# Kernel optimization log

Hardware: AMD Instinct MI355X
Metric: run time of the kernel (lower is better)

## Reference

```python
import jax, jax.numpy as jnp
import numpy as np

B, LQ, LK, H, DK, DV, E = 4, 1024, 1024, 12, 64, 768, 768
TOPK = 64
TEMP = 0.5
NEG = -10000.0


def setup_inputs() -> dict:
    key = jax.random.key(0)
    ks = jax.random.split(key, 10)
    s = 0.02  # weight init scale
    return {
        "q": jax.random.normal(ks[0], (B, LQ, E), jnp.float32),
        "k": jax.random.normal(ks[1], (B, LK, E), jnp.float32),
        "v": jax.random.normal(ks[2], (B, LK, DV), jnp.float32),
        "qpos": jnp.zeros((B, LQ), jnp.int32),
        "kpos": jnp.zeros((B, LK), jnp.int32),
        "qk_mask": jax.random.normal(ks[3], (B, 1, LQ, LK), jnp.float32) * 0.1,
        "k_mask": jax.random.normal(ks[4], (B, 1, LK, 1), jnp.float32) * 0.1,
        "post_softmax_mask": (jax.random.uniform(ks[5], (B, 1, LQ, LK)) > 0.1).astype(jnp.float32),
        "w_qs": jax.random.normal(ks[6], (E, H * DK), jnp.float32) * s,
        "w_ks": jax.random.normal(ks[7], (E, H * DK), jnp.float32) * s,
        "w_vs": jax.random.normal(ks[8], (DV, H * DV), jnp.float32) * s,
        "fc": jax.random.normal(ks[9], (H * DV, DV), jnp.float32) * s,
    }


def reference(q, k, v, qpos, kpos, qk_mask, k_mask, post_softmax_mask, w_qs, w_ks, w_vs, fc):
    residual = v
    # project and split heads: [b, len, h, d] -> [b, h, len, d]
    qh = (q @ w_qs).reshape(B, LQ, H, DK).transpose(0, 2, 1, 3)
    kh = (k @ w_ks).reshape(B, LK, H, DK).transpose(0, 2, 1, 3)
    vh = (v @ w_vs).reshape(B, LK, H, DV).transpose(0, 2, 1, 3)

    # scaled dot-product scores [b, h, lq, lk]
    attn = jnp.einsum('bhqd,bhkd->bhqk', qh / np.float32(np.sqrt(DK)), kh)
    attn = attn + qk_mask                              # additive qk mask
    attn = attn + jnp.squeeze(k_mask, -1)[:, :, None, :]  # additive key mask

    # topk sparsification: keep top-k scores, fill rest with -10000
    topk_vals, topk_idx = jax.lax.top_k(attn, TOPK)
    attn = jnp.put_along_axis(jnp.full_like(attn, NEG), topk_idx, topk_vals,
                              axis=-1, inplace=False)

    # temperature + stable softmax in fp32
    attn = attn / max(TEMP, 1e-6)
    attn = jax.nn.softmax(attn.astype(jnp.float32), axis=-1).astype(v.dtype)

    # post-softmax multiplicative mask + renorm (renorm_post_mask=True)
    attn = attn * post_softmax_mask
    attn = attn / jnp.maximum(attn.sum(axis=-1, keepdims=True), 1e-6)

    # straight-through argmax hardening (use_argmax=True)
    hard = jax.nn.one_hot(jnp.argmax(attn, axis=-1), LK, dtype=attn.dtype)
    attn = hard - jax.lax.stop_gradient(attn) + attn

    # attend, merge heads, output projection + residual (dropout=0)
    head_output = jnp.einsum('bhqk,bhkd->bhqd', attn, vh)
    output = head_output.transpose(0, 2, 1, 3).reshape(B, LQ, H * DV) @ fc
    output = output + residual
    return (output, attn)
```

## Files before the change

kernel.cpp:

```cpp
#include <hip/hip_runtime.h>

constexpr int NB  = 4;
constexpr int NH  = 12;
constexpr int SEQ = 1024;
constexpr int DKd = 64;
constexpr int DVd = 768;
constexpr int Ed  = 768;
constexpr int HVd = 9216;

typedef float f32x4 __attribute__((ext_vector_type(4)));
typedef short s16x8 __attribute__((ext_vector_type(8)));

__device__ __forceinline__ unsigned short f2bf(float f) {
  unsigned int u = __builtin_bit_cast(unsigned int, f);
  u += 0x7fffu + ((u >> 16) & 1u);
  return (unsigned short)(u >> 16);
}

__device__ __forceinline__ float bf2f_lo(unsigned int u) {
  return __builtin_bit_cast(float, u << 16);
}
__device__ __forceinline__ float bf2f_hi(unsigned int u) {
  return __builtin_bit_cast(float, u & 0xffff0000u);
}

__device__ __forceinline__ f32x4 mfma_bf16_16x16x32(s16x8 a, s16x8 b, f32x4 c) {
  asm("v_mfma_f32_16x16x32_bf16 %0, %1, %2, %0" : "+v"(c) : "v"(a), "v"(b));
  return c;
}

#define GLOAD16(g, l)                                                          \
  __builtin_amdgcn_global_load_lds(                                            \
      (const __attribute__((address_space(1))) unsigned int*)(g),              \
      (__attribute__((address_space(3))) unsigned int*)(l), 16, 0, 0)

__global__ __launch_bounds__(256)
void cvt_bf16_kernel(const float* __restrict__ v, unsigned short* __restrict__ Vbf, int n4) {
  int i = blockIdx.x * 256 + threadIdx.x;
  const int stride = gridDim.x * 256;
  for (; i < n4; i += stride) {
    const f32x4 x = *(const f32x4*)&v[(size_t)i * 4];
    uint2 u;
    u.x = (unsigned)f2bf(x[0]) | ((unsigned)f2bf(x[1]) << 16);
    u.y = (unsigned)f2bf(x[2]) | ((unsigned)f2bf(x[3]) << 16);
    *(uint2*)&Vbf[(size_t)i * 4] = u;
  }
}

__global__ __launch_bounds__(256)
void maskprep_kernel(const float* __restrict__ qk, const float* __restrict__ km,
                     const float* __restrict__ pm, float* __restrict__ ms) {
  const int i = blockIdx.x * 256 + threadIdx.x;
  const int kk4 = i & 255;
  const int b = i >> 18;
  const f32x4 qv = *(const f32x4*)&qk[(size_t)i * 4];
  const f32x4 pv = *(const f32x4*)&pm[(size_t)i * 4];
  const f32x4 kv = *(const f32x4*)&km[b * SEQ + kk4 * 4];
  f32x4 o;
#pragma unroll
  for (int c = 0; c < 4; c++) o[c] = pv[c] > 0.f ? qv[c] + kv[c] : -3.0e38f;
  *(f32x4*)&ms[(size_t)i * 4] = o;
}

__global__ __launch_bounds__(256)
void qkproj_kernel(const float* __restrict__ q, const float* __restrict__ k,
                   const float* __restrict__ w_qs, const float* __restrict__ w_ks,
                   float* __restrict__ qh, float* __restrict__ kh) {
  const float* A  = blockIdx.z ? k : q;
  const float* Bw = blockIdx.z ? w_ks : w_qs;
  float* C        = blockIdx.z ? kh : qh;
  __shared__ float As[16][128];
  __shared__ float Bs[16][128];
  const int tid = threadIdx.x;
  const int bx = (int)blockIdx.x;
  const int sx = ((bx & 7) << 2) | (bx >> 3);
  const int m0 = sx * 128, n0 = blockIdx.y * 128;
  const int ty = tid >> 4, tx = tid & 15;
  const int arow = tid >> 1, akc = (tid & 1) * 8;
  const int bkr = tid >> 4, bnc = (tid & 15) * 8;

  float acc[8][8];
#pragma unroll
  for (int i = 0; i < 8; i++)
#pragma unroll
    for (int j = 0; j < 8; j++) acc[i][j] = 0.f;

  for (int k0 = 0; k0 < 768; k0 += 16) {
    const f32x4 av0 = *(const f32x4*)&A[(size_t)(m0 + arow) * 768 + k0 + akc];
    const f32x4 av1 = *(const f32x4*)&A[(size_t)(m0 + arow) * 768 + k0 + akc + 4];
    const f32x4 bv0 = *(const f32x4*)&Bw[(size_t)(k0 + bkr) * 768 + n0 + bnc];
    const f32x4 bv1 = *(const f32x4*)&Bw[(size_t)(k0 + bkr) * 768 + n0 + bnc + 4];
    __syncthreads();
#pragma unroll
    for (int c = 0; c < 4; c++) {
      As[akc + c][arow]     = av0[c];
      As[akc + 4 + c][arow] = av1[c];
    }
    *(f32x4*)&Bs[bkr][bnc]     = bv0;
    *(f32x4*)&Bs[bkr][bnc + 4] = bv1;
    __syncthreads();
#pragma unroll
    for (int kk = 0; kk < 16; kk++) {
      const f32x4 a0 = *(const f32x4*)&As[kk][ty * 8];
      const f32x4 a1 = *(const f32x4*)&As[kk][ty * 8 + 4];
      const f32x4 b0 = *(const f32x4*)&Bs[kk][tx * 8];
      const f32x4 b1 = *(const f32x4*)&Bs[kk][tx * 8 + 4];
#pragma unroll
      for (int i = 0; i < 4; i++)
#pragma unroll
        for (int j = 0; j < 4; j++) {
          acc[i][j]         += a0[i] * b0[j];
          acc[i][j + 4]     += a0[i] * b1[j];
          acc[i + 4][j]     += a1[i] * b0[j];
          acc[i + 4][j + 4] += a1[i] * b1[j];
        }
    }
  }
#pragma unroll
  for (int i = 0; i < 8; i++) {
    f32x4 o0, o1;
#pragma unroll
    for (int c = 0; c < 4; c++) { o0[c] = acc[i][c]; o1[c] = acc[i][4 + c]; }
    const size_t rb = (size_t)(m0 + ty * 8 + i) * 768 + n0 + tx * 8;
    *(f32x4*)&C[rb] = o0;
    *(f32x4*)&C[rb + 4] = o1;
  }
}

__global__ __launch_bounds__(256)
void score_argmax_kernel(const float* __restrict__ qh, const float* __restrict__ kh,
                         const float* __restrict__ ms, float2* __restrict__ partials) {
  __shared__ float QsT[64][128];
  __shared__ float KsT[64][128];
  const int bh = blockIdx.z;
  const int b = bh / NH, h = bh % NH;
  const int q0 = blockIdx.y * 128;
  const int k0 = blockIdx.x * 128;
  const int tid = threadIdx.x;
  const int ty = tid >> 4, tx = tid & 15;

  const int row = tid >> 1;
  const int cb = (tid & 1) * 32;
  const float* qsrc = qh + (size_t)(b * SEQ + q0 + row) * Ed + h * DKd + cb;
  const float* ksrc = kh + (size_t)(b * SEQ + k0 + row) * Ed + h * DKd + cb;
#pragma unroll
  for (int i = 0; i < 8; i++) {
    const f32x4 qv = *(const f32x4*)&qsrc[4 * i];
    const f32x4 kv = *(const f32x4*)&ksrc[4 * i];
#pragma unroll
    for (int c = 0; c < 4; c++) {
      QsT[cb + 4 * i + c][row] = qv[c];
      KsT[cb + 4 * i + c][row] = kv[c];
    }
  }
  __syncthreads();

  float acc[8][8];
#pragma unroll
  for (int i = 0; i < 8; i++)
#pragma unroll
    for (int j = 0; j < 8; j++) acc[i][j] = 0.f;

#pragma unroll 8
  for (int kk = 0; kk < 64; kk++) {
    const f32x4 a0 = *(const f32x4*)&QsT[kk][ty * 8];
    const f32x4 a1 = *(const f32x4*)&QsT[kk][ty * 8 + 4];
    const f32x4 b0 = *(const f32x4*)&KsT[kk][tx * 8];
    const f32x4 b1 = *(const f32x4*)&KsT[kk][tx * 8 + 4];
#pragma unroll
    for (int i = 0; i < 4; i++)
#pragma unroll
      for (int j = 0; j < 4; j++) {
        acc[i][j]         += a0[i] * b0[j];
        acc[i][j + 4]     += a0[i] * b1[j];
        acc[i + 4][j]     += a1[i] * b0[j];
        acc[i + 4][j + 4] += a1[i] * b1[j];
      }
  }

  const int kg0 = k0 + tx * 8;
#pragma unroll
  for (int i = 0; i < 8; i++) {
    const int qg = q0 + ty * 8 + i;
    const size_t base = (size_t)(b * SEQ + qg) * SEQ + kg0;
    const f32x4 ms0 = *(const f32x4*)&ms[base];
    const f32x4 ms1 = *(const f32x4*)&ms[base + 4];
    float bv = -3.0e38f;
    int bi = 0;
#pragma unroll
    for (int j = 0; j < 4; j++) {
      const float s = acc[i][j] * 0.125f + ms0[j];
      if (s > bv) { bv = s; bi = kg0 + j; }
    }
#pragma unroll
    for (int j = 0; j < 4; j++) {
      const float s = acc[i][4 + j] * 0.125f + ms1[j];
      if (s > bv) { bv = s; bi = kg0 + 4 + j; }
    }
#pragma unroll
    for (int off = 1; off < 16; off <<= 1) {
      const float ov = __shfl_xor(bv, off);
      const int   oi = __shfl_xor(bi, off);
      if (ov > bv || (ov == bv && oi < bi)) { bv = ov; bi = oi; }
    }
    if (tx == 0)
      partials[(size_t)(bh * SEQ + qg) * 8 + blockIdx.x] =
          make_float2(bv, __int_as_float(bi));
  }
}

__global__ __launch_bounds__(256)
void argmax_reduce_kernel(const float2* __restrict__ partials, int* __restrict__ kmaxp) {
  const int t = blockIdx.x * 256 + threadIdx.x;
  if (t >= NB * NH * SEQ) return;
  const float2* p = partials + (size_t)t * 8;
  float bv = -3.0e38f;
  int bi = 0;
#pragma unroll
  for (int i = 0; i < 8; i++) {
    const float vv = p[i].x;
    const int ii = __float_as_int(p[i].y);
    if (vv > bv) { bv = vv; bi = ii; }
  }
  kmaxp[t] = bi;
}

__global__ __launch_bounds__(256)
void wvfc_gemm_kernel(const float* __restrict__ wvs, const float* __restrict__ fcw,
                      unsigned short* __restrict__ MstbT) {
  __shared__ unsigned short As[128][72];
  __shared__ unsigned short Bs[128][72];
  const int tid = threadIdx.x;
  const int h = blockIdx.z;
  const int m0 = blockIdx.x * 128, n0 = blockIdx.y * 128;
  const int wid = tid >> 6, lane = tid & 63;
  const int wr = (wid >> 1) * 64, wc = (wid & 1) * 64;
  const int lm = lane & 15, lq = lane >> 4;
  const int ar = tid >> 1, acb = (tid & 1) * 32;
  const int br = tid >> 2, bnb = (tid & 3) * 32;

  f32x4 acc[4][4];
#pragma unroll
  for (int m = 0; m < 4; m++)
#pragma unroll
    for (int n = 0; n < 4; n++)
#pragma unroll
      for (int r = 0; r < 4; r++) acc[m][n][r] = 0.f;

  for (int k0 = 0; k0 < 768; k0 += 64) {
    const float* asrc = wvs + (size_t)(m0 + ar) * HVd + h * 768 + k0 + acb;
    const float* bsrc = fcw + (size_t)(h * 768 + k0 + br) * 768 + n0 + bnb;
    f32x4 a4[8], b4[8];
#pragma unroll
    for (int i = 0; i < 8; i++) a4[i] = *(const f32x4*)&asrc[4 * i];
#pragma unroll
    for (int i = 0; i < 8; i++) b4[i] = *(const f32x4*)&bsrc[4 * i];
    __syncthreads();
#pragma unroll
    for (int i = 0; i < 4; i++) {
      s16x8 pk;
#pragma unroll
      for (int j = 0; j < 8; j++) pk[j] = (short)f2bf(a4[2 * i + (j >> 2)][j & 3]);
      *(s16x8*)&As[ar][acb + 8 * i] = pk;
    }
#pragma unroll
    for (int i = 0; i < 8; i++)
#pragma unroll
      for (int c = 0; c < 4; c++) Bs[bnb + 4 * i + c][br] = f2bf(b4[i][c]);
    __syncthreads();
#pragma unroll
    for (int ks = 0; ks < 2; ks++) {
      s16x8 af[4], bfr[4];
#pragma unroll
      for (int m = 0; m < 4; m++)
        af[m] = *(const s16x8*)&As[wr + m * 16 + lm][ks * 32 + lq * 8];
#pragma unroll
      for (int n = 0; n < 4; n++)
        bfr[n] = *(const s16x8*)&Bs[wc + n * 16 + lm][ks * 32 + lq * 8];
#pragma unroll
      for (int m = 0; m < 4; m++)
#pragma unroll
        for (int n = 0; n < 4; n++)
          acc[m][n] = mfma_bf16_16x16x32(af[m], bfr[n], acc[m][n]);
    }
  }
  asm volatile("s_nop 7\n\ts_nop 7");
#pragma unroll
  for (int m = 0; m < 4; m++)
#pragma unroll
    for (int n = 0; n < 4; n++) {
      const int grow0 = m0 + wr + m * 16 + lq * 4;
      const int gcol  = n0 + wc + n * 16 + lm;
      uint2 u;
      u.x = (unsigned)f2bf(acc[m][n][0]) | ((unsigned)f2bf(acc[m][n][1]) << 16);
      u.y = (unsigned)f2bf(acc[m][n][2]) | ((unsigned)f2bf(acc[m][n][3]) << 16);
      *(uint2*)&MstbT[(size_t)(h * 768 + gcol) * 768 + grow0] = u;
    }
}

__global__ __launch_bounds__(256)
void ugemm_kernel(const unsigned short* __restrict__ Vbf,
                  const unsigned short* __restrict__ MstbT,
                  unsigned short* __restrict__ U, int h0) {
  __shared__ unsigned short As[128 * 64];
  __shared__ unsigned short Bs[128 * 64];
  const int tid = threadIdx.x;
  const int h = h0 + blockIdx.z;
  const int bx = (int)blockIdx.x;
  const int sx = ((bx & 7) << 2) | (bx >> 3);
  const int m0 = sx * 128, n0 = blockIdx.y * 128;
  const int wid = tid >> 6, lane = tid & 63;
  const int wr = (wid >> 1) * 64, wc = (wid & 1) * 64;
  const int lm = lane & 15, lq = lane >> 4;
  const int srow = tid >> 3, scol = (tid & 7) * 8;
  const int ldst = (tid >> 6) * 512;

  const unsigned short* asrc = Vbf + (size_t)(m0 + srow) * 768 + scol;
  const unsigned short* bsrc = MstbT + (size_t)(h * 768 + n0 + srow) * 768 + scol;

  f32x4 acc[4][4];
#pragma unroll
  for (int m = 0; m < 4; m++)
#pragma unroll
    for (int n = 0; n < 4; n++)
#pragma unroll
      for (int r = 0; r < 4; r++) acc[m][n][r] = 0.f;

  for (int k0 = 0; k0 < 768; k0 += 64) {
#pragma unroll
    for (int j = 0; j < 4; j++)
      GLOAD16(asrc + (size_t)j * 32 * 768 + k0, &As[j * 2048 + ldst]);
#pragma unroll
    for (int j = 0; j < 4; j++)
      GLOAD16(bsrc + (size_t)j * 32 * 768 + k0, &Bs[j * 2048 + ldst]);
    __syncthreads();
#pragma unroll
    for (int ks = 0; ks < 2; ks++) {
      s16x8 af[4], bfr[4];
#pragma unroll
      for (int m = 0; m < 4; m++)
        af[m] = *(const s16x8*)&As[(wr + m * 16 + lm) * 64 + ks * 32 + lq * 8];
#pragma unroll
      for (int n = 0; n < 4; n++)
        bfr[n] = *(const s16x8*)&Bs[(wc + n * 16 + lm) * 64 + ks * 32 + lq * 8];
#pragma unroll
      for (int m = 0; m < 4; m++)
#pragma unroll
        for (int n = 0; n < 4; n++)
          acc[m][n] = mfma_bf16_16x16x32(af[m], bfr[n], acc[m][n]);
    }
    __syncthreads();
  }
  asm volatile("s_nop 7\n\ts_nop 7");
  const size_t urow0 = (size_t)blockIdx.z * 4096;
#pragma unroll
  for (int m = 0; m < 4; m++)
#pragma unroll
    for (int r = 0; r < 4; r++) {
      const int row = m0 + wr + m * 16 + lq * 4 + r;
      uint2 u;
      u.x = (unsigned)f2bf(acc[m][0][r]) | ((unsigned)f2bf(acc[m][1][r]) << 16);
      u.y = (unsigned)f2bf(acc[m][2][r]) | ((unsigned)f2bf(acc[m][3][r]) << 16);
      *(uint2*)&U[(urow0 + row) * 768 + n0 + wc + lm * 4] = u;
    }
}

__global__ __launch_bounds__(192)
void gathersum_kernel(const unsigned short* __restrict__ U, const int* __restrict__ kmaxp,
                      const float* __restrict__ v, float* __restrict__ out0, int h0) {
  const int row = blockIdx.x;
  const int b = row >> 10, q = row & 1023;
  const int t = threadIdx.x;
  float a0 = 0.f, a1 = 0.f, a2 = 0.f, a3 = 0.f;
#pragma unroll
  for (int hg = 0; hg < 6; hg++) {
    const int g = kmaxp[((b * NH + h0 + hg) << 10) + q];
    const uint2 u = *(const uint2*)&U[((size_t)hg * 4096 + (b << 10) + g) * 768 + t * 4];
    a0 += bf2f_lo(u.x);
    a1 += bf2f_hi(u.x);
    a2 += bf2f_lo(u.y);
    a3 += bf2f_hi(u.y);
  }
  const int chunk = t >> 4, lmm = t & 15;
  const size_t ob = (size_t)row * 768 + chunk * 64 + lmm;
  if (h0 == 0) {
    out0[ob +  0] = a0 + v[ob +  0];
    out0[ob + 16] = a1 + v[ob + 16];
    out0[ob + 32] = a2 + v[ob + 32];
    out0[ob + 48] = a3 + v[ob + 48];
  } else {
    out0[ob +  0] += a0;
    out0[ob + 16] += a1;
    out0[ob + 32] += a2;
    out0[ob + 48] += a3;
  }
}

__global__ void zero_kernel(f32x4* __restrict__ p, int n4) {
  int i = blockIdx.x * blockDim.x + threadIdx.x;
  const int stride = gridDim.x * blockDim.x;
  f32x4 z;
  z[0] = z[1] = z[2] = z[3] = 0.f;
  for (; i < n4; i += stride) p[i] = z;
}

__global__ __launch_bounds__(256)
void scatter_kernel(const int* __restrict__ kmaxp, float* __restrict__ attn) {
  const int t = blockIdx.x * 256 + threadIdx.x;
  if (t >= NB * NH * SEQ) return;
  attn[((size_t)t << 10) + kmaxp[t]] = 1.0f;
}

extern "C" void kernel_launch(void* const* d_in, const int* in_sizes, int n_in,
                              void* d_out, int out_size, void* d_ws, size_t ws_size,
                              hipStream_t stream) {
  (void)in_sizes; (void)n_in; (void)out_size; (void)ws_size;
  const float* q       = (const float*)d_in[0];
  const float* k       = (const float*)d_in[1];
  const float* v       = (const float*)d_in[2];
  const float* qk_mask = (const float*)d_in[5];
  const float* k_mask  = (const float*)d_in[6];
  const float* pmask   = (const float*)d_in[7];
  const float* w_qs    = (const float*)d_in[8];
  const float* w_ks    = (const float*)d_in[9];
  const float* w_vs    = (const float*)d_in[10];
  const float* fc      = (const float*)d_in[11];

  float* out0 = (float*)d_out;
  float* attn = out0 + (size_t)NB * SEQ * DVd;

  char* ws = (char*)d_ws;
  unsigned short* MstbT = (unsigned short*)ws;
  unsigned short* Vbf   = (unsigned short*)(ws + 14155776);
  float* msbuf          = (float*)ws;
  int* kmaxp            = (int*)(ws + 20447232);
  char* ureg            = ws + 20643840;
  unsigned short* U     = (unsigned short*)ureg;
  float* qh             = (float*)ureg;
  float* kh             = (float*)(ureg + 12582912);
  float2* partials      = (float2*)(ureg + 25165824);

  maskprep_kernel<<<dim3(4096), 256, 0, stream>>>(qk_mask, k_mask, pmask, msbuf);

  qkproj_kernel<<<dim3(32, 6, 2), 256, 0, stream>>>(q, k, w_qs, w_ks, qh, kh);

  score_argmax_kernel<<<dim3(8, 8, NB * NH), 256, 0, stream>>>(qh, kh, msbuf, partials);
  argmax_reduce_kernel<<<dim3((NB * NH * SEQ + 255) / 256), 256, 0, stream>>>(partials, kmaxp);

  cvt_bf16_kernel<<<dim3(3072), 256, 0, stream>>>(v, Vbf, NB * SEQ * DVd / 4);

  wvfc_gemm_kernel<<<dim3(6, 6, NH), 256, 0, stream>>>(w_vs, fc, MstbT);

  ugemm_kernel<<<dim3(32, 6, 6), 256, 0, stream>>>(Vbf, MstbT, U, 0);
  gathersum_kernel<<<dim3(NB * SEQ), 192, 0, stream>>>(U, kmaxp, v, out0, 0);
  ugemm_kernel<<<dim3(32, 6, 6), 256, 0, stream>>>(Vbf, MstbT, U, 6);
  gathersum_kernel<<<dim3(NB * SEQ), 192, 0, stream>>>(U, kmaxp, v, out0, 6);

  zero_kernel<<<dim3(2048), 256, 0, stream>>>((f32x4*)attn,
                                              (int)((size_t)NB * NH * SEQ * SEQ / 4));
  scatter_kernel<<<dim3((NB * NH * SEQ + 255) / 256), 256, 0, stream>>>(kmaxp, attn);
}
```

Before: 473.9 us.

## Loop heads inside score kernel, fuse one-hot write, single-pass U GEMM when workspace allows

The score/argmax kernel now processes all 12 heads per block, loading the mask tile into shared memory once and reusing it across heads instead of re-reading it from global memory per head. The QK projection uses narrower 128x64 tiles with more blocks and drops the block swizzle. The attn output is written in one pass that emits the one-hot directly, replacing a zero-fill kernel followed by a scatter. When the workspace is large enough, the value GEMM and gather run once over all 12 heads instead of in two halves. These changes cut mask traffic and launches, at the cost of a serial head loop per block and lower arithmetic intensity in the projection GEMM.

```diff
diff --git a/kernel.cpp b/kernel.cpp
--- a/kernel.cpp
+++ b/kernel.cpp
@@ -70,142 +70,143 @@
   const float* Bw = blockIdx.z ? w_ks : w_qs;
   float* C        = blockIdx.z ? kh : qh;
   __shared__ float As[16][128];
-  __shared__ float Bs[16][128];
+  __shared__ float Bs[16][64];
   const int tid = threadIdx.x;
-  const int bx = (int)blockIdx.x;
-  const int sx = ((bx & 7) << 2) | (bx >> 3);
-  const int m0 = sx * 128, n0 = blockIdx.y * 128;
+  const int m0 = blockIdx.x * 128, n0 = blockIdx.y * 64;
   const int ty = tid >> 4, tx = tid & 15;
   const int arow = tid >> 1, akc = (tid & 1) * 8;
-  const int bkr = tid >> 4, bnc = (tid & 15) * 8;
-
-  float acc[8][8];
+  const int bkr = tid >> 4, bnc = (tid & 15) * 4;
+
+  float acc[8][4];
 #pragma unroll
   for (int i = 0; i < 8; i++)
 #pragma unroll
-    for (int j = 0; j < 8; j++) acc[i][j] = 0.f;
+    for (int j = 0; j < 4; j++) acc[i][j] = 0.f;
 
   for (int k0 = 0; k0 < 768; k0 += 16) {
     const f32x4 av0 = *(const f32x4*)&A[(size_t)(m0 + arow) * 768 + k0 + akc];
     const f32x4 av1 = *(const f32x4*)&A[(size_t)(m0 + arow) * 768 + k0 + akc + 4];
-    const f32x4 bv0 = *(const f32x4*)&Bw[(size_t)(k0 + bkr) * 768 + n0 + bnc];
-    const f32x4 bv1 = *(const f32x4*)&Bw[(size_t)(k0 + bkr) * 768 + n0 + bnc + 4];
+    const f32x4 bv  = *(const f32x4*)&Bw[(size_t)(k0 + bkr) * 768 + n0 + bnc];
     __syncthreads();
 #pragma unroll
     for (int c = 0; c < 4; c++) {
       As[akc + c][arow]     = av0[c];
       As[akc + 4 + c][arow] = av1[c];
     }
-    *(f32x4*)&Bs[bkr][bnc]     = bv0;
-    *(f32x4*)&Bs[bkr][bnc + 4] = bv1;
+    *(f32x4*)&Bs[bkr][bnc] = bv;
     __syncthreads();
 #pragma unroll
     for (int kk = 0; kk < 16; kk++) {
       const f32x4 a0 = *(const f32x4*)&As[kk][ty * 8];
       const f32x4 a1 = *(const f32x4*)&As[kk][ty * 8 + 4];
-      const f32x4 b0 = *(const f32x4*)&Bs[kk][tx * 8];
-      const f32x4 b1 = *(const f32x4*)&Bs[kk][tx * 8 + 4];
+      const f32x4 b  = *(const f32x4*)&Bs[kk][tx * 4];
 #pragma unroll
       for (int i = 0; i < 4; i++)
 #pragma unroll
         for (int j = 0; j < 4; j++) {
-          acc[i][j]         += a0[i] * b0[j];
-          acc[i][j + 4]     += a0[i] * b1[j];
-          acc[i + 4][j]     += a1[i] * b0[j];
-          acc[i + 4][j + 4] += a1[i] * b1[j];
+          acc[i][j]     += a0[i] * b[j];
+          acc[i + 4][j] += a1[i] * b[j];
         }
     }
   }
 #pragma unroll
   for (int i = 0; i < 8; i++) {
-    f32x4 o0, o1;
-#pragma unroll
-    for (int c = 0; c < 4; c++) { o0[c] = acc[i][c]; o1[c] = acc[i][4 + c]; }
-    const size_t rb = (size_t)(m0 + ty * 8 + i) * 768 + n0 + tx * 8;
-    *(f32x4*)&C[rb] = o0;
-    *(f32x4*)&C[rb + 4] = o1;
+    f32x4 o;
+#pragma unroll
+    for (int j = 0; j < 4; j++) o[j] = acc[i][j];
+    *(f32x4*)&C[(size_t)(m0 + ty * 8 + i) * 768 + n0 + tx * 4] = o;
   }
 }
 
 __global__ __launch_bounds__(256)
 void score_argmax_kernel(const float* __restrict__ qh, const float* __restrict__ kh,
                          const float* __restrict__ ms, float2* __restrict__ partials) {
-  __shared__ float QsT[64][128];
+  __shared__ float msS[64][128];
+  __shared__ float QsT[64][64];
   __shared__ float KsT[64][128];
-  const int bh = blockIdx.z;
-  const int b = bh / NH, h = bh % NH;
-  const int q0 = blockIdx.y * 128;
+  const int b  = blockIdx.z;
+  const int q0 = blockIdx.y * 64;
   const int k0 = blockIdx.x * 128;
   const int tid = threadIdx.x;
   const int ty = tid >> 4, tx = tid & 15;
 
-  const int row = tid >> 1;
-  const int cb = (tid & 1) * 32;
-  const float* qsrc = qh + (size_t)(b * SEQ + q0 + row) * Ed + h * DKd + cb;
-  const float* ksrc = kh + (size_t)(b * SEQ + k0 + row) * Ed + h * DKd + cb;
-#pragma unroll
-  for (int i = 0; i < 8; i++) {
-    const f32x4 qv = *(const f32x4*)&qsrc[4 * i];
-    const f32x4 kv = *(const f32x4*)&ksrc[4 * i];
-#pragma unroll
-    for (int c = 0; c < 4; c++) {
-      QsT[cb + 4 * i + c][row] = qv[c];
-      KsT[cb + 4 * i + c][row] = kv[c];
-    }
-  }
-  __syncthreads();
-
-  float acc[8][8];
-#pragma unroll
-  for (int i = 0; i < 8; i++)
-#pragma unroll
-    for (int j = 0; j < 8; j++) acc[i][j] = 0.f;
+  {
+    const int row = tid >> 2, cc = (tid & 3) * 32;
+    const float* src = ms + (size_t)(b * SEQ + q0 + row) * SEQ + k0 + cc;
+#pragma unroll
+    for (int i = 0; i < 8; i++)
+      *(f32x4*)&msS[row][cc + 4 * i] = *(const f32x4*)&src[4 * i];
+  }
+
+  const int qr = tid >> 2, qdc = (tid & 3) * 16;
+  const int kr = tid >> 1, kdc = (tid & 1) * 32;
+  const float* qbase = qh + (size_t)(b * SEQ + q0 + qr) * Ed + qdc;
+  const float* kbase = kh + (size_t)(b * SEQ + k0 + kr) * Ed + kdc;
+  const int kg0 = k0 + tx * 8;
+
+  for (int h = 0; h < NH; h++) {
+    __syncthreads();
+#pragma unroll
+    for (int j = 0; j < 4; j++) {
+      const f32x4 qv = *(const f32x4*)&qbase[h * 64 + 4 * j];
+#pragma unroll
+      for (int c = 0; c < 4; c++) QsT[qdc + 4 * j + c][qr] = qv[c];
+    }
+#pragma unroll
+    for (int j = 0; j < 8; j++) {
+      const f32x4 kv = *(const f32x4*)&kbase[h * 64 + 4 * j];
+#pragma unroll
+      for (int c = 0; c < 4; c++) KsT[kdc + 4 * j + c][kr] = kv[c];
+    }
+    __syncthreads();
+
+    float acc[4][8];
+#pragma unroll
+    for (int i = 0; i < 4; i++)
+#pragma unroll
+      for (int j = 0; j < 8; j++) acc[i][j] = 0.f;
 
 #pragma unroll 8
-  for (int kk = 0; kk < 64; kk++) {
-    const f32x4 a0 = *(const f32x4*)&QsT[kk][ty * 8];
-    const f32x4 a1 = *(const f32x4*)&QsT[kk][ty * 8 + 4];
-    const f32x4 b0 = *(const f32x4*)&KsT[kk][tx * 8];
-    const f32x4 b1 = *(const f32x4*)&KsT[kk][tx * 8 + 4];
-#pragma unroll
-    for (int i = 0; i < 4; i++)
+    for (int kk = 0; kk < 64; kk++) {
+      const f32x4 qf  = *(const f32x4*)&QsT[kk][ty * 4];
+      const f32x4 kf0 = *(const f32x4*)&KsT[kk][tx * 8];
+      const f32x4 kf1 = *(const f32x4*)&KsT[kk][tx * 8 + 4];
+#pragma unroll
+      for (int i = 0; i < 4; i++)
+#pragma unroll
+        for (int j = 0; j < 4; j++) {
+          acc[i][j]     += qf[i] * kf0[j];
+          acc[i][j + 4] += qf[i] * kf1[j];
+        }
+    }
+
+#pragma unroll
+    for (int i = 0; i < 4; i++) {
+      const int qg = q0 + ty * 4 + i;
+      const f32x4 m0v = *(const f32x4*)&msS[ty * 4 + i][tx * 8];
+      const f32x4 m1v = *(const f32x4*)&msS[ty * 4 + i][tx * 8 + 4];
+      float bv = -3.0e38f;
+      int bi = 0;
 #pragma unroll
       for (int j = 0; j < 4; j++) {
-        acc[i][j]         += a0[i] * b0[j];
-        acc[i][j + 4]     += a0[i] * b1[j];
-        acc[i + 4][j]     += a1[i] * b0[j];
-        acc[i + 4][j + 4] += a1[i] * b1[j];
+        const float s = acc[i][j] * 0.125f + m0v[j];
+        if (s > bv) { bv = s; bi = kg0 + j; }
       }
-  }
-
-  const int kg0 = k0 + tx * 8;
-#pragma unroll
-  for (int i = 0; i < 8; i++) {
-    const int qg = q0 + ty * 8 + i;
-    const size_t base = (size_t)(b * SEQ + qg) * SEQ + kg0;
-    const f32x4 ms0 = *(const f32x4*)&ms[base];
-    const f32x4 ms1 = *(const f32x4*)&ms[base + 4];
-    float bv = -3.0e38f;
-    int bi = 0;
-#pragma unroll
-    for (int j = 0; j < 4; j++) {
-      const float s = acc[i][j] * 0.125f + ms0[j];
-      if (s > bv) { bv = s; bi = kg0 + j; }
-    }
-#pragma unroll
-    for (int j = 0; j < 4; j++) {
-      const float s = acc[i][4 + j] * 0.125f + ms1[j];
-      if (s > bv) { bv = s; bi = kg0 + 4 + j; }
-    }
-#pragma unroll
-    for (int off = 1; off < 16; off <<= 1) {
-      const float ov = __shfl_xor(bv, off);
-      const int   oi = __shfl_xor(bi, off);
-      if (ov > bv || (ov == bv && oi < bi)) { bv = ov; bi = oi; }
-    }
-    if (tx == 0)
-      partials[(size_t)(bh * SEQ + qg) * 8 + blockIdx.x] =
-          make_float2(bv, __int_as_float(bi));
+#pragma unroll
+      for (int j = 0; j < 4; j++) {
+        const float s = acc[i][4 + j] * 0.125f + m1v[j];
+        if (s > bv) { bv = s; bi = kg0 + 4 + j; }
+      }
+#pragma unroll
+      for (int off = 1; off < 16; off <<= 1) {
+        const float ov = __shfl_xor(bv, off);
+        const int   oi = __shfl_xor(bi, off);
+        if (ov > bv || (ov == bv && oi < bi)) { bv = ov; bi = oi; }
+      }
+      if (tx == 0)
+        partials[(size_t)((b * NH + h) * SEQ + qg) * 8 + blockIdx.x] =
+            make_float2(bv, __int_as_float(bi));
+    }
   }
 }
 
@@ -367,13 +368,13 @@
 
 __global__ __launch_bounds__(192)
 void gathersum_kernel(const unsigned short* __restrict__ U, const int* __restrict__ kmaxp,
-                      const float* __restrict__ v, float* __restrict__ out0, int h0) {
+                      const float* __restrict__ v, float* __restrict__ out0,
+                      int h0, int nhg) {
   const int row = blockIdx.x;
   const int b = row >> 10, q = row & 1023;
   const int t = threadIdx.x;
   float a0 = 0.f, a1 = 0.f, a2 = 0.f, a3 = 0.f;
-#pragma unroll
-  for (int hg = 0; hg < 6; hg++) {
+  for (int hg = 0; hg < nhg; hg++) {
     const int g = kmaxp[((b * NH + h0 + hg) << 10) + q];
     const uint2 u = *(const uint2*)&U[((size_t)hg * 4096 + (b << 10) + g) * 768 + t * 4];
     a0 += bf2f_lo(u.x);
@@ -396,25 +397,24 @@
   }
 }
 
-__global__ void zero_kernel(f32x4* __restrict__ p, int n4) {
+__global__ void onehot_kernel(const int* __restrict__ kmaxp, f32x4* __restrict__ attn, int n4) {
   int i = blockIdx.x * blockDim.x + threadIdx.x;
   const int stride = gridDim.x * blockDim.x;
-  f32x4 z;
-  z[0] = z[1] = z[2] = z[3] = 0.f;
-  for (; i < n4; i += stride) p[i] = z;
-}
-
-__global__ __launch_bounds__(256)
-void scatter_kernel(const int* __restrict__ kmaxp, float* __restrict__ attn) {
-  const int t = blockIdx.x * 256 + threadIdx.x;
-  if (t >= NB * NH * SEQ) return;
-  attn[((size_t)t << 10) + kmaxp[t]] = 1.0f;
+  for (; i < n4; i += stride) {
+    const int row = i >> 8;
+    const int c0 = (i & 255) * 4;
+    const int km = kmaxp[row];
+    f32x4 o;
+#pragma unroll
+    for (int c = 0; c < 4; c++) o[c] = (c0 + c == km) ? 1.0f : 0.0f;
+    attn[i] = o;
+  }
 }
 
 extern "C" void kernel_launch(void* const* d_in, const int* in_sizes, int n_in,
                               void* d_out, int out_size, void* d_ws, size_t ws_size,
                               hipStream_t stream) {
-  (void)in_sizes; (void)n_in; (void)out_size; (void)ws_size;
+  (void)in_sizes; (void)n_in; (void)out_size;
   const float* q       = (const float*)d_in[0];
   const float* k       = (const float*)d_in[1];
   const float* v       = (const float*)d_in[2];
@@ -440,23 +440,29 @@
   float* kh             = (float*)(ureg + 12582912);
   float2* partials      = (float2*)(ureg + 25165824);
 
+  const bool big = ws_size >= (size_t)96141312;
+
   maskprep_kernel<<<dim3(4096), 256, 0, stream>>>(qk_mask, k_mask, pmask, msbuf);
 
-  qkproj_kernel<<<dim3(32, 6, 2), 256, 0, stream>>>(q, k, w_qs, w_ks, qh, kh);
-
-  score_argmax_kernel<<<dim3(8, 8, NB * NH), 256, 0, stream>>>(qh, kh, msbuf, partials);
+  qkproj_kernel<<<dim3(32, 12, 2), 256, 0, stream>>>(q, k, w_qs, w_ks, qh, kh);
+
+  score_argmax_kernel<<<dim3(8, 16, NB), 256, 0, stream>>>(qh, kh, msbuf, partials);
   argmax_reduce_kernel<<<dim3((NB * NH * SEQ + 255) / 256), 256, 0, stream>>>(partials, kmaxp);
 
   cvt_bf16_kernel<<<dim3(3072), 256, 0, stream>>>(v, Vbf, NB * SEQ * DVd / 4);
 
   wvfc_gemm_kernel<<<dim3(6, 6, NH), 256, 0, stream>>>(w_vs, fc, MstbT);
 
-  ugemm_kernel<<<dim3(32, 6, 6), 256, 0, stream>>>(Vbf, MstbT, U, 0);
-  gathersum_kernel<<<dim3(NB * SEQ), 192, 0, stream>>>(U, kmaxp, v, out0, 0);
-  ugemm_kernel<<<dim3(32, 6, 6), 256, 0, stream>>>(Vbf, MstbT, U, 6);
-  gathersum_kernel<<<dim3(NB * SEQ), 192, 0, stream>>>(U, kmaxp, v, out0, 6);
-
-  zero_kernel<<<dim3(2048), 256, 0, stream>>>((f32x4*)attn,
-                                              (int)((size_t)NB * NH * SEQ * SEQ / 4));
-  scatter_kernel<<<dim3((NB * NH * SEQ + 255) / 256), 256, 0, stream>>>(kmaxp, attn);
-}
+  if (big) {
+    ugemm_kernel<<<dim3(32, 6, 12), 256, 0, stream>>>(Vbf, MstbT, U, 0);
+    gathersum_kernel<<<dim3(NB * SEQ), 192, 0, stream>>>(U, kmaxp, v, out0, 0, 12);
+  } else {
+    ugemm_kernel<<<dim3(32, 6, 6), 256, 0, stream>>>(Vbf, MstbT, U, 0);
+    gathersum_kernel<<<dim3(NB * SEQ), 192, 0, stream>>>(U, kmaxp, v, out0, 0, 6);
+    ugemm_kernel<<<dim3(32, 6, 6), 256, 0, stream>>>(Vbf, MstbT, U, 6);
+    gathersum_kernel<<<dim3(NB * SEQ), 192, 0, stream>>>(U, kmaxp, v, out0, 6, 6);
+  }
+
+  onehot_kernel<<<dim3(2048), 256, 0, stream>>>(kmaxp, (f32x4*)attn,
+                                                (int)((size_t)NB * NH * SEQ * SEQ / 4));
+}
```

Result: faster. 452.7 us (-4.5%).
